# Performance work log

Measured on AMD Instinct MI355X. Metric: run time of the kernel, lower is better.

## Reference

```python
import jax, jax.numpy as jnp
import numpy as np
import math

EMBED_DIM = 128

def setup_inputs() -> dict:
    key = jax.random.key(0)
    ks = jax.random.split(key, 5)
    b, n, k, d = 4, 8192, 16, EMBED_DIM
    src = jax.random.normal(ks[0], (b, n, d), dtype=jnp.float32)
    tgt = jax.random.normal(ks[1], (b, n, k, d), dtype=jnp.float32)
    # Linear(d, d, bias=False) weights; torch applies x @ W.T
    s = 1.0 / math.sqrt(d)
    Wq = jax.random.uniform(ks[2], (d, d), dtype=jnp.float32, minval=-s, maxval=s)
    Wk = jax.random.uniform(ks[3], (d, d), dtype=jnp.float32, minval=-s, maxval=s)
    Wv = jax.random.uniform(ks[4], (d, d), dtype=jnp.float32, minval=-s, maxval=s)
    return {"src": src, "tgt": tgt, "Wq": Wq, "Wk": Wk, "Wv": Wv}

def reference(src, tgt, Wq, Wk, Wv):
    d = src.shape[-1]
    scale = 1.0 / math.sqrt(d)
    Q = src @ Wq.T                     # [b,n,d]
    K = tgt @ Wk.T                     # [b,n,k,d]
    V = tgt @ Wv.T                     # [b,n,k,d]
    scores = jnp.einsum('bnkd,bnd->bnk', K, Q) * scale  # [b,n,k]
    attn = jax.nn.softmax(scores, axis=-1)
    return jnp.einsum('bnk,bnkd->bnd', attn, V)          # [b,n,d]
```

## Files before the change

kernel.cpp:

```cpp
#include <hip/hip_runtime.h>
#include <math.h>

#define D 128
#define KTGT 16

__global__ void prep_kernel(const float* __restrict__ Wq,
                            const float* __restrict__ Wk,
                            const float* __restrict__ Wv,
                            float* __restrict__ Wqk,
                            float* __restrict__ WvT) {
    const int drow = blockIdx.x;
    const int c    = threadIdx.x;
    float acc = 0.0f;
    #pragma unroll 8
    for (int j = 0; j < D; ++j)
        acc = fmaf(Wq[j * D + drow], Wk[j * D + c], acc);
    Wqk[drow * D + c] = acc;
    WvT[drow * D + c] = Wv[c * D + drow];
}

__global__ __launch_bounds__(256) void rowgemm_kernel(const float* __restrict__ A,
                                                      const float* __restrict__ B,
                                                      float* __restrict__ C) {
    __shared__ float Alds[32][D];
    const int r0 = blockIdx.x * 32;
    {
        const float4* Ag = reinterpret_cast<const float4*>(A + (size_t)r0 * D);
        float4* Al = reinterpret_cast<float4*>(&Alds[0][0]);
        #pragma unroll
        for (int i = 0; i < 4; ++i)
            Al[threadIdx.x + i * 256] = Ag[threadIdx.x + i * 256];
    }
    __syncthreads();

    const int cblk = threadIdx.x & 31;
    const int rblk = threadIdx.x >> 5;
    float acc[4][4] = {};
    const float4* B4 = reinterpret_cast<const float4*>(B);

    for (int d0 = 0; d0 < D; d0 += 4) {
        float4 a[4];
        #pragma unroll
        for (int j = 0; j < 4; ++j)
            a[j] = *reinterpret_cast<const float4*>(&Alds[rblk * 4 + j][d0]);
        #pragma unroll
        for (int dd = 0; dd < 4; ++dd) {
            float4 w = B4[(d0 + dd) * 32 + cblk];
            #pragma unroll
            for (int j = 0; j < 4; ++j) {
                float aj = (&a[j].x)[dd];
                acc[j][0] = fmaf(aj, w.x, acc[j][0]);
                acc[j][1] = fmaf(aj, w.y, acc[j][1]);
                acc[j][2] = fmaf(aj, w.z, acc[j][2]);
                acc[j][3] = fmaf(aj, w.w, acc[j][3]);
            }
        }
    }

    #pragma unroll
    for (int j = 0; j < 4; ++j) {
        float4 o = make_float4(acc[j][0], acc[j][1], acc[j][2], acc[j][3]);
        *reinterpret_cast<float4*>(C + (size_t)(r0 + rblk * 4 + j) * D + cblk * 4) = o;
    }
}

__global__ __launch_bounds__(256) void attn_kernel(const float* __restrict__ tgt,
                                                   float* __restrict__ SC,
                                                   int nrows) {
    const int lane = threadIdx.x & 63;
    const int wid  = (int)((blockIdx.x * blockDim.x + threadIdx.x) >> 6);
    const int nw   = (int)((gridDim.x * blockDim.x) >> 6);
    const int d4   = lane & 31;
    const float scale = 0.088388347648318447f;

    for (int r = wid; r < nrows; r += nw) {
        float4 Sv = *reinterpret_cast<const float4*>(SC + (size_t)r * D + d4 * 4);
        const float4* T4 = reinterpret_cast<const float4*>(tgt + (size_t)r * KTGT * D);

        float4 tv[8];
        float p[8];
        #pragma unroll
        for (int i = 0; i < 8; ++i) {
            tv[i] = T4[i * 64 + lane];
            p[i] = tv[i].x * Sv.x + tv[i].y * Sv.y + tv[i].z * Sv.z + tv[i].w * Sv.w;
        }
        #pragma unroll
        for (int m = 1; m <= 16; m <<= 1) {
            #pragma unroll
            for (int i = 0; i < 8; ++i)
                p[i] += __shfl_xor(p[i], m, 64);
        }
        float q[8];
        #pragma unroll
        for (int i = 0; i < 8; ++i) {
            p[i] *= scale;
            q[i] = __shfl_xor(p[i], 32, 64);
        }
        float mx = -1e30f;
        #pragma unroll
        for (int i = 0; i < 8; ++i) mx = fmaxf(mx, fmaxf(p[i], q[i]));
        float sum = 0.0f;
        float ep[8];
        #pragma unroll
        for (int i = 0; i < 8; ++i) {
            ep[i] = __expf(p[i] - mx);
            float eq = __expf(q[i] - mx);
            sum += ep[i] + eq;
        }
        const float inv = 1.0f / sum;
        float cx = 0.f, cy = 0.f, cz = 0.f, cw = 0.f;
        #pragma unroll
        for (int i = 0; i < 8; ++i) {
            float w = ep[i] * inv;
            cx = fmaf(w, tv[i].x, cx);
            cy = fmaf(w, tv[i].y, cy);
            cz = fmaf(w, tv[i].z, cz);
            cw = fmaf(w, tv[i].w, cw);
        }
        cx += __shfl_xor(cx, 32, 64);
        cy += __shfl_xor(cy, 32, 64);
        cz += __shfl_xor(cz, 32, 64);
        cw += __shfl_xor(cw, 32, 64);
        if (lane < 32) {
            float4 o = make_float4(cx, cy, cz, cw);
            *reinterpret_cast<float4*>(SC + (size_t)r * D + d4 * 4) = o;
        }
    }
}

extern "C" void kernel_launch(void* const* d_in, const int* in_sizes, int n_in,
                              void* d_out, int out_size, void* d_ws, size_t ws_size,
                              hipStream_t stream) {
    const float* src = (const float*)d_in[0];
    const float* tgt = (const float*)d_in[1];
    const float* Wq  = (const float*)d_in[2];
    const float* Wk  = (const float*)d_in[3];
    const float* Wv  = (const float*)d_in[4];
    float* out = (float*)d_out;

    float* Wqk = (float*)d_ws;
    float* WvT = Wqk + D * D;

    const int nrows = in_sizes[0] / D;

    prep_kernel<<<D, D, 0, stream>>>(Wq, Wk, Wv, Wqk, WvT);
    rowgemm_kernel<<<nrows / 32, 256, 0, stream>>>(src, Wqk, out);
    attn_kernel<<<2048, 256, 0, stream>>>(tgt, out, nrows);
    rowgemm_kernel<<<nrows / 32, 256, 0, stream>>>(out, WvT, out);
}
```

Before: 434.0 us.

## Fuse Q projection, attention and V projection into one per-row persistent kernel

Replaces the two row-GEMM launches and the attention kernel with one persistent kernel. Each 512-thread block walks a contiguous run of rows and keeps slices of the folded Wq·Wk and transposed Wv matrices in registers. For every row it computes the projected query, the 16 scores, the softmax and the context sum, then applies the V projection. This avoids writing the intermediate results to global memory and reading them back, and it drops two launches. The next row's tgt and src are prefetched, but only one row per block is in flight and each row needs four block-wide barriers, so memory-level parallelism may fall well short of the old grid-stride attention kernel.

```diff
diff --git a/kernel.cpp b/kernel.cpp
--- a/kernel.cpp
+++ b/kernel.cpp
@@ -19,112 +19,136 @@
     WvT[drow * D + c] = Wv[c * D + drow];
 }
 
-__global__ __launch_bounds__(256) void rowgemm_kernel(const float* __restrict__ A,
-                                                      const float* __restrict__ B,
-                                                      float* __restrict__ C) {
-    __shared__ float Alds[32][D];
-    const int r0 = blockIdx.x * 32;
-    {
-        const float4* Ag = reinterpret_cast<const float4*>(A + (size_t)r0 * D);
-        float4* Al = reinterpret_cast<float4*>(&Alds[0][0]);
-        #pragma unroll
-        for (int i = 0; i < 4; ++i)
-            Al[threadIdx.x + i * 256] = Ag[threadIdx.x + i * 256];
+__global__ __launch_bounds__(512, 2) void fused_kernel(
+        const float* __restrict__ src, const float* __restrict__ tgt,
+        const float* __restrict__ Wqk, const float* __restrict__ WvT,
+        float* __restrict__ out, int nrows) {
+    __shared__ __align__(16) float SrcS[D];
+    __shared__ __align__(16) float Sbuf[D];
+    __shared__ __align__(16) float Scs[KTGT];
+    __shared__ __align__(16) float CtxP[8][D];
+    __shared__ __align__(16) float Ctx[D];
+
+    const int tid  = threadIdx.x;
+    const int w    = tid >> 6;
+    const int lane = tid & 63;
+    const int h    = lane >> 5;
+    const int q    = lane & 31;
+    const int cl   = lane & 15;
+    const int g    = (lane >> 4) & 3;
+    const int col  = w * 16 + cl;
+    const int myk  = 2 * w + h;
+    const float scale = 0.088388347648318447f;
+
+    float Wq_r[32], Wv_r[32];
+    #pragma unroll
+    for (int j = 0; j < 32; ++j) {
+        Wq_r[j] = Wqk[(size_t)(g * 32 + j) * D + col];
+        Wv_r[j] = WvT[(size_t)(g * 32 + j) * D + col];
     }
+
+    const int rpb = (nrows + gridDim.x - 1) / gridDim.x;
+    const int r0  = blockIdx.x * rpb;
+
+    if (r0 < nrows) {
+        if (tid < 32)
+            ((float4*)SrcS)[tid] = ((const float4*)(src + (size_t)r0 * D))[tid];
+    }
+    float4 tv = make_float4(0.f, 0.f, 0.f, 0.f);
+    if (r0 < nrows)
+        tv = ((const float4*)(tgt + (size_t)r0 * (KTGT * D)))[myk * 32 + q];
     __syncthreads();
 
-    const int cblk = threadIdx.x & 31;
-    const int rblk = threadIdx.x >> 5;
-    float acc[4][4] = {};
-    const float4* B4 = reinterpret_cast<const float4*>(B);
+    for (int i = 0; i < rpb; ++i) {
+        const int r = r0 + i;
+        if (r >= nrows) break;
 
-    for (int d0 = 0; d0 < D; d0 += 4) {
-        float4 a[4];
+        float sS = 0.f;
         #pragma unroll
-        for (int j = 0; j < 4; ++j)
-            a[j] = *reinterpret_cast<const float4*>(&Alds[rblk * 4 + j][d0]);
-        #pragma unroll
-        for (int dd = 0; dd < 4; ++dd) {
-            float4 w = B4[(d0 + dd) * 32 + cblk];
-            #pragma unroll
-            for (int j = 0; j < 4; ++j) {
-                float aj = (&a[j].x)[dd];
-                acc[j][0] = fmaf(aj, w.x, acc[j][0]);
-                acc[j][1] = fmaf(aj, w.y, acc[j][1]);
-                acc[j][2] = fmaf(aj, w.z, acc[j][2]);
-                acc[j][3] = fmaf(aj, w.w, acc[j][3]);
-            }
+        for (int jb = 0; jb < 8; ++jb) {
+            float4 s4 = *(const float4*)&SrcS[g * 32 + jb * 4];
+            sS = fmaf(s4.x, Wq_r[jb * 4 + 0], sS);
+            sS = fmaf(s4.y, Wq_r[jb * 4 + 1], sS);
+            sS = fmaf(s4.z, Wq_r[jb * 4 + 2], sS);
+            sS = fmaf(s4.w, Wq_r[jb * 4 + 3], sS);
         }
-    }
+        sS += __shfl_xor(sS, 16, 64);
+        sS += __shfl_xor(sS, 32, 64);
+        if ((lane >> 4) == 0) Sbuf[col] = sS;
+        __syncthreads();
 
-    #pragma unroll
-    for (int j = 0; j < 4; ++j) {
-        float4 o = make_float4(acc[j][0], acc[j][1], acc[j][2], acc[j][3]);
-        *reinterpret_cast<float4*>(C + (size_t)(r0 + rblk * 4 + j) * D + cblk * 4) = o;
-    }
-}
+        float4 Sv = *(const float4*)&Sbuf[q * 4];
+        float p = tv.x * Sv.x + tv.y * Sv.y + tv.z * Sv.z + tv.w * Sv.w;
+        p += __shfl_xor(p, 1, 64);
+        p += __shfl_xor(p, 2, 64);
+        p += __shfl_xor(p, 4, 64);
+        p += __shfl_xor(p, 8, 64);
+        p += __shfl_xor(p, 16, 64);
+        const float myp = p * scale;
+        if (q == 0) Scs[myk] = myp;
 
-__global__ __launch_bounds__(256) void attn_kernel(const float* __restrict__ tgt,
-                                                   float* __restrict__ SC,
-                                                   int nrows) {
-    const int lane = threadIdx.x & 63;
-    const int wid  = (int)((blockIdx.x * blockDim.x + threadIdx.x) >> 6);
-    const int nw   = (int)((gridDim.x * blockDim.x) >> 6);
-    const int d4   = lane & 31;
-    const float scale = 0.088388347648318447f;
+        const bool more = (i + 1 < rpb) && (r + 1 < nrows);
+        const int rn = more ? (r + 1) : r;
+        float4 tvn = ((const float4*)(tgt + (size_t)rn * (KTGT * D)))[myk * 32 + q];
+        if (more && w == 1 && lane < 32)
+            ((float4*)SrcS)[lane] = ((const float4*)(src + (size_t)(r + 1) * D))[lane];
+        __syncthreads();
 
-    for (int r = wid; r < nrows; r += nw) {
-        float4 Sv = *reinterpret_cast<const float4*>(SC + (size_t)r * D + d4 * 4);
-        const float4* T4 = reinterpret_cast<const float4*>(tgt + (size_t)r * KTGT * D);
+        float4 sc0 = *(const float4*)&Scs[0];
+        float4 sc1 = *(const float4*)&Scs[4];
+        float4 sc2 = *(const float4*)&Scs[8];
+        float4 sc3 = *(const float4*)&Scs[12];
+        float mx = fmaxf(fmaxf(fmaxf(sc0.x, sc0.y), fmaxf(sc0.z, sc0.w)),
+                         fmaxf(fmaxf(fmaxf(sc1.x, sc1.y), fmaxf(sc1.z, sc1.w)),
+                               fmaxf(fmaxf(fmaxf(sc2.x, sc2.y), fmaxf(sc2.z, sc2.w)),
+                                     fmaxf(fmaxf(sc3.x, sc3.y), fmaxf(sc3.z, sc3.w)))));
+        float sum =
+            __expf(sc0.x - mx) + __expf(sc0.y - mx) + __expf(sc0.z - mx) + __expf(sc0.w - mx) +
+            __expf(sc1.x - mx) + __expf(sc1.y - mx) + __expf(sc1.z - mx) + __expf(sc1.w - mx) +
+            __expf(sc2.x - mx) + __expf(sc2.y - mx) + __expf(sc2.z - mx) + __expf(sc2.w - mx) +
+            __expf(sc3.x - mx) + __expf(sc3.y - mx) + __expf(sc3.z - mx) + __expf(sc3.w - mx);
+        const float a = __expf(myp - mx) / sum;
 
-        float4 tv[8];
-        float p[8];
-        #pragma unroll
-        for (int i = 0; i < 8; ++i) {
-            tv[i] = T4[i * 64 + lane];
-            p[i] = tv[i].x * Sv.x + tv[i].y * Sv.y + tv[i].z * Sv.z + tv[i].w * Sv.w;
-        }
-        #pragma unroll
-        for (int m = 1; m <= 16; m <<= 1) {
-            #pragma unroll
-            for (int i = 0; i < 8; ++i)
-                p[i] += __shfl_xor(p[i], m, 64);
-        }
-        float q[8];
-        #pragma unroll
-        for (int i = 0; i < 8; ++i) {
-            p[i] *= scale;
-            q[i] = __shfl_xor(p[i], 32, 64);
-        }
-        float mx = -1e30f;
-        #pragma unroll
-        for (int i = 0; i < 8; ++i) mx = fmaxf(mx, fmaxf(p[i], q[i]));
-        float sum = 0.0f;
-        float ep[8];
-        #pragma unroll
-        for (int i = 0; i < 8; ++i) {
-            ep[i] = __expf(p[i] - mx);
-            float eq = __expf(q[i] - mx);
-            sum += ep[i] + eq;
-        }
-        const float inv = 1.0f / sum;
-        float cx = 0.f, cy = 0.f, cz = 0.f, cw = 0.f;
-        #pragma unroll
-        for (int i = 0; i < 8; ++i) {
-            float w = ep[i] * inv;
-            cx = fmaf(w, tv[i].x, cx);
-            cy = fmaf(w, tv[i].y, cy);
-            cz = fmaf(w, tv[i].z, cz);
-            cw = fmaf(w, tv[i].w, cw);
-        }
+        float cx = a * tv.x, cy = a * tv.y, cz = a * tv.z, cw = a * tv.w;
         cx += __shfl_xor(cx, 32, 64);
         cy += __shfl_xor(cy, 32, 64);
         cz += __shfl_xor(cz, 32, 64);
         cw += __shfl_xor(cw, 32, 64);
-        if (lane < 32) {
-            float4 o = make_float4(cx, cy, cz, cw);
-            *reinterpret_cast<float4*>(SC + (size_t)r * D + d4 * 4) = o;
+        if (h == 0) *((float4*)&CtxP[w][q * 4]) = make_float4(cx, cy, cz, cw);
+        __syncthreads();
+
+        if (tid < 32) {
+            float4 t0 = *(const float4*)&CtxP[0][tid * 4];
+            float4 t1 = *(const float4*)&CtxP[1][tid * 4];
+            float4 t2 = *(const float4*)&CtxP[2][tid * 4];
+            float4 t3 = *(const float4*)&CtxP[3][tid * 4];
+            float4 t4 = *(const float4*)&CtxP[4][tid * 4];
+            float4 t5 = *(const float4*)&CtxP[5][tid * 4];
+            float4 t6 = *(const float4*)&CtxP[6][tid * 4];
+            float4 t7 = *(const float4*)&CtxP[7][tid * 4];
+            float4 tt;
+            tt.x = ((t0.x + t1.x) + (t2.x + t3.x)) + ((t4.x + t5.x) + (t6.x + t7.x));
+            tt.y = ((t0.y + t1.y) + (t2.y + t3.y)) + ((t4.y + t5.y) + (t6.y + t7.y));
+            tt.z = ((t0.z + t1.z) + (t2.z + t3.z)) + ((t4.z + t5.z) + (t6.z + t7.z));
+            tt.w = ((t0.w + t1.w) + (t2.w + t3.w)) + ((t4.w + t5.w) + (t6.w + t7.w));
+            *((float4*)&Ctx[tid * 4]) = tt;
         }
+        __syncthreads();
+
+        float sO = 0.f;
+        #pragma unroll
+        for (int jb = 0; jb < 8; ++jb) {
+            float4 c4 = *(const float4*)&Ctx[g * 32 + jb * 4];
+            sO = fmaf(c4.x, Wv_r[jb * 4 + 0], sO);
+            sO = fmaf(c4.y, Wv_r[jb * 4 + 1], sO);
+            sO = fmaf(c4.z, Wv_r[jb * 4 + 2], sO);
+            sO = fmaf(c4.w, Wv_r[jb * 4 + 3], sO);
+        }
+        sO += __shfl_xor(sO, 16, 64);
+        sO += __shfl_xor(sO, 32, 64);
+        if ((lane >> 4) == 0) out[(size_t)r * D + col] = sO;
+
+        tv = tvn;
     }
 }
 
@@ -144,7 +168,5 @@
     const int nrows = in_sizes[0] / D;
 
     prep_kernel<<<D, D, 0, stream>>>(Wq, Wk, Wv, Wqk, WvT);
-    rowgemm_kernel<<<nrows / 32, 256, 0, stream>>>(src, Wqk, out);
-    attn_kernel<<<2048, 256, 0, stream>>>(tgt, out, nrows);
-    rowgemm_kernel<<<nrows / 32, 256, 0, stream>>>(out, WvT, out);
+    fused_kernel<<<256, 512, 0, stream>>>(src, tgt, Wqk, WvT, out, nrows);
 }
```

New measurement: 580.3 us. +33.7%, slower.
